# Optimization experiments

Measured on AMD Instinct MI355X. Metric: run time of the kernel, lower is better.

## Reference

```python
import jax, jax.numpy as jnp
import numpy as np

NUM_CLASSES = 80
GRID = 13
A = 9                      # 3 scales x 3 anchors, flattened
P = GRID * GRID * A        # 1521 priors
OBJ_SCALE, NOOBJ_SCALE, CLS_SCALE, BOX_SCALE = 1.0, 100.0, 1.0, 5.0
ANCHORS_NP = np.array([[10,13],[16,30],[33,23],[30,61],[62,45],[59,119],[116,90],[156,198],[373,326]], dtype=np.float32)


def setup_inputs() -> dict:
    key = jax.random.key(0)
    k1, k2, k3, k4, k5 = jax.random.split(key, 5)
    B, T = 512, 50
    predictions = jax.random.normal(k1, (B, P, 5 + NUM_CLASSES), dtype=jnp.float32)
    xy = jax.random.uniform(k2, (B, T, 2), minval=0.02, maxval=0.98)
    wh = jax.random.uniform(k3, (B, T, 2), minval=0.01, maxval=0.30)
    conf = (jax.random.uniform(k4, (B, T, 1)) < 0.6).astype(jnp.float32)
    cls = jax.random.randint(k5, (B, T, 1), 0, NUM_CLASSES).astype(jnp.float32)
    targets = jnp.concatenate([xy, wh, conf, cls], axis=-1)  # [B,T,6]
    anchors = jnp.asarray(ANCHORS_NP)                        # [9,2]
    return {"predictions": predictions, "targets": targets, "anchors": anchors}


def _safe_log(x):
    # torch BCELoss clamps log terms at -100
    return jnp.maximum(jnp.log(x), -100.0)


def _per_image(pred, tgt, anchors):
    # pred: [P, 5+C], tgt: [T, 6], anchors: [A, 2]
    valid = tgt[:, 4] > 0
    has = jnp.any(valid)
    # wh-only IoU: target wh scaled by 1000 (pixel scale) vs anchor wh
    tw_px = tgt[:, 2] * 1000.0
    th_px = tgt[:, 3] * 1000.0
    aw = anchors[:, 0][:, None]  # [A,1]
    ah = anchors[:, 1][:, None]
    inter = jnp.minimum(aw, tw_px[None, :]) * jnp.minimum(ah, th_px[None, :])  # [A,T]
    union = aw * ah + tw_px * th_px - inter
    iou = inter / (union + 1e-16)
    best_a = jnp.argmax(iou, axis=0)  # [T]
    gx = jnp.floor(tgt[:, 0] * GRID).astype(jnp.int32)
    gy = jnp.floor(tgt[:, 1] * GRID).astype(jnp.int32)
    prior = gy * (GRID * A) + gx * A + best_a
    prior = jnp.where(valid, prior, P)  # invalid targets scatter out-of-range -> dropped

    obj = jnp.zeros((P,), jnp.float32).at[prior].set(1.0, mode='drop')
    txv = tgt[:, 0] * GRID - gx.astype(jnp.float32)
    tyv = tgt[:, 1] * GRID - gy.astype(jnp.float32)
    aw_b = anchors[best_a, 0]
    ah_b = anchors[best_a, 1]
    twv = jnp.log(tgt[:, 2] * GRID / aw_b + 1e-16)
    thv = jnp.log(tgt[:, 3] * GRID / ah_b + 1e-16)
    tx = jnp.zeros((P,), jnp.float32).at[prior].set(txv, mode='drop')
    ty = jnp.zeros((P,), jnp.float32).at[prior].set(tyv, mode='drop')
    tw = jnp.zeros((P,), jnp.float32).at[prior].set(twv, mode='drop')
    th = jnp.zeros((P,), jnp.float32).at[prior].set(thv, mode='drop')
    cls_idx = tgt[:, 5].astype(jnp.int32)
    tcls = jnp.zeros((P, NUM_CLASSES), jnp.float32).at[prior, cls_idx].set(1.0, mode='drop')

    conf_p = jax.nn.sigmoid(pred[:, 4])
    logp = _safe_log(conf_p)
    log1mp = _safe_log(1.0 - conf_p)

    box = BOX_SCALE * jnp.sum(obj * ((pred[:, 0] - tx) ** 2 + (pred[:, 1] - ty) ** 2
                                     + (pred[:, 2] - tw) ** 2 + (pred[:, 3] - th) ** 2))
    objl = -OBJ_SCALE * jnp.sum(obj * logp)
    # empty-image branch: BCE(conf, ones).sum() = -sum(log p); otherwise BCE over noobj priors vs 0
    noobjl = jnp.where(has,
                       -NOOBJ_SCALE * jnp.sum((1.0 - obj) * log1mp),
                       -NOOBJ_SCALE * jnp.sum(logp))
    pcls = jax.nn.sigmoid(pred[:, 5:])
    bce_cls = -(tcls * _safe_log(pcls) + (1.0 - tcls) * _safe_log(1.0 - pcls))
    clsl = CLS_SCALE * jnp.sum(obj[:, None] * bce_cls)
    return box, objl, noobjl, clsl


def reference(predictions, targets, anchors):
    box, objl, noobjl, clsl = jax.vmap(lambda p, t: _per_image(p, t, anchors))(predictions, targets)
    B = predictions.shape[0]
    box_loss = jnp.sum(box) / B
    obj_loss = jnp.sum(objl) / B
    noobj_loss = jnp.sum(noobjl) / B
    cls_loss = jnp.sum(clsl) / B
    total = box_loss + obj_loss + noobj_loss + cls_loss
    return (total, box_loss, obj_loss, noobj_loss, cls_loss)
```

## Files before the change

kernel.cpp:

```cpp
#include <hip/hip_runtime.h>
#include <cmath>

#define B_N 512
#define T_N 50
#define GRIDN 13
#define A_N 9
#define P_N 1521
#define ROW 85
#define NCLS 80

struct Entry {
    int prior;
    float tx, ty, tw, th;
    unsigned int cls[3];
};

__global__ void __launch_bounds__(256)
main_kernel(const float* __restrict__ pred,
            const float* __restrict__ tgt,
            const float* __restrict__ anchors,
            float* __restrict__ part)
{
    __shared__ Entry ents[T_N];
    __shared__ int   s_cnt;
    __shared__ float red[4][5];

    const int tid  = threadIdx.x;
    const int lane = tid & 63;
    const int b    = blockIdx.x;

    if (tid < 64) {
        int   prior = -1;
        float txv = 0.f, tyv = 0.f, twv = 0.f, thv = 0.f;
        int   cls = 0;

        if (lane < T_N) {
            const float* t = tgt + ((size_t)b * T_N + lane) * 6;
            float x = t[0], y = t[1], w = t[2], h = t[3], conf = t[4];
            if (conf > 0.0f) {
                float tw_px = w * 1000.0f, th_px = h * 1000.0f;
                int best = 0; float bestv = -1.0f;
                #pragma unroll
                for (int a = 0; a < A_N; ++a) {
                    float aw = anchors[2*a], ah = anchors[2*a+1];
                    float inter = fminf(aw, tw_px) * fminf(ah, th_px);
                    float uni   = aw*ah + tw_px*th_px - inter;
                    float iou   = inter / (uni + 1e-16f);
                    if (iou > bestv) { bestv = iou; best = a; }
                }
                int gx = (int)floorf(x * (float)GRIDN);
                int gy = (int)floorf(y * (float)GRIDN);
                prior = gy * (GRIDN * A_N) + gx * A_N + best;
                txv = x * (float)GRIDN - (float)gx;
                tyv = y * (float)GRIDN - (float)gy;
                float aw = anchors[2*best], ah = anchors[2*best+1];
                twv = logf(w * (float)GRIDN / aw + 1e-16f);
                thv = logf(h * (float)GRIDN / ah + 1e-16f);
                cls = (int)t[5];
            }
        }

        bool valid = (prior >= 0);
        unsigned int m0 = 0, m1 = 0, m2 = 0;
        bool laterdup = false;
        #pragma unroll
        for (int j = 0; j < T_N; ++j) {
            int pj = __shfl(prior, j, 64);
            int cj = __shfl(cls,   j, 64);
            if (valid && pj == prior) {
                if (j > lane) laterdup = true;
                if (cj < 32)      m0 |= 1u << cj;
                else if (cj < 64) m1 |= 1u << (cj - 32);
                else              m2 |= 1u << (cj - 64);
            }
        }
        bool winner = valid && !laterdup;
        unsigned long long mask = __ballot(winner);
        if (winner) {
            int idx = __popcll(mask & ((1ull << lane) - 1ull));
            Entry* e = &ents[idx];
            e->prior = prior;
            e->tx = txv; e->ty = tyv; e->tw = twv; e->th = thv;
            e->cls[0] = m0; e->cls[1] = m1; e->cls[2] = m2;
        }
        if (lane == 0) s_cnt = __popcll(mask);
    }
    __syncthreads();

    const int  cnt  = s_cnt;
    const bool hasv = (cnt > 0);

    const float* pb = pred + (size_t)b * P_N * ROW;
    float s_main = 0.0f;
    #pragma unroll
    for (int p = tid; p < P_N; p += 256) {
        float x = pb[(size_t)p * ROW + 4];
        float s = 1.0f / (1.0f + __expf(-x));
        float v = hasv ? fmaxf(__logf(1.0f - s), -100.0f)
                       : fmaxf(__logf(s),        -100.0f);
        s_main += v;
    }

    float cls_s = 0.0f, box_s = 0.0f, objlp = 0.0f, objl1 = 0.0f;
    {
        const int half = tid >> 7;
        const int lt   = tid & 127;
        for (int e = half; e < cnt; e += 2) {
            Entry en = ents[e];
            const float* row = pb + (size_t)en.prior * ROW;
            if (lt < NCLS) {
                float x  = row[5 + lt];
                float s  = 1.0f / (1.0f + __expf(-x));
                float lp = fmaxf(__logf(s),        -100.0f);
                float l1 = fmaxf(__logf(1.0f - s), -100.0f);
                float tc = ((en.cls[lt >> 5] >> (lt & 31)) & 1u) ? 1.0f : 0.0f;
                cls_s += -(tc * lp + (1.0f - tc) * l1);
            } else if (lt == NCLS) {
                float x = row[4];
                float s = 1.0f / (1.0f + __expf(-x));
                objlp += fmaxf(__logf(s),        -100.0f);
                objl1 += fmaxf(__logf(1.0f - s), -100.0f);
            } else if (lt == NCLS + 1) {
                float d0 = row[0] - en.tx;
                float d1 = row[1] - en.ty;
                float d2 = row[2] - en.tw;
                float d3 = row[3] - en.th;
                box_s += d0*d0 + d1*d1 + d2*d2 + d3*d3;
            }
        }
    }

    float v0 = s_main, v1 = objl1, v2 = objlp, v3 = box_s, v4 = cls_s;
    #pragma unroll
    for (int o = 32; o > 0; o >>= 1) {
        v0 += __shfl_down(v0, o, 64);
        v1 += __shfl_down(v1, o, 64);
        v2 += __shfl_down(v2, o, 64);
        v3 += __shfl_down(v3, o, 64);
        v4 += __shfl_down(v4, o, 64);
    }
    const int w = tid >> 6;
    if (lane == 0) {
        red[w][0] = v0; red[w][1] = v1; red[w][2] = v2;
        red[w][3] = v3; red[w][4] = v4;
    }
    __syncthreads();
    if (tid == 0) {
        float S  = red[0][0] + red[1][0] + red[2][0] + red[3][0];
        float L1 = red[0][1] + red[1][1] + red[2][1] + red[3][1];
        float LP = red[0][2] + red[1][2] + red[2][2] + red[3][2];
        float BX = red[0][3] + red[1][3] + red[2][3] + red[3][3];
        float CL = red[0][4] + red[1][4] + red[2][4] + red[3][4];
        float* o = part + (size_t)b * 4;
        o[0] = 5.0f * BX;
        o[1] = -LP;
        o[2] = -100.0f * (S - L1);
        o[3] = CL;
    }
}

__global__ void __launch_bounds__(256)
finalize_kernel(const float* __restrict__ part, float* __restrict__ out)
{
    __shared__ float red[4][4];
    const int tid  = threadIdx.x;
    const int lane = tid & 63;

    float a0 = 0, a1 = 0, a2 = 0, a3 = 0;
    for (int b = tid; b < B_N; b += 256) {
        const float* p = part + (size_t)b * 4;
        a0 += p[0]; a1 += p[1]; a2 += p[2]; a3 += p[3];
    }
    #pragma unroll
    for (int o = 32; o > 0; o >>= 1) {
        a0 += __shfl_down(a0, o, 64);
        a1 += __shfl_down(a1, o, 64);
        a2 += __shfl_down(a2, o, 64);
        a3 += __shfl_down(a3, o, 64);
    }
    const int w = tid >> 6;
    if (lane == 0) { red[w][0] = a0; red[w][1] = a1; red[w][2] = a2; red[w][3] = a3; }
    __syncthreads();
    if (tid == 0) {
        const float invB = 1.0f / (float)B_N;
        float box   = (red[0][0] + red[1][0] + red[2][0] + red[3][0]) * invB;
        float obj   = (red[0][1] + red[1][1] + red[2][1] + red[3][1]) * invB;
        float noobj = (red[0][2] + red[1][2] + red[2][2] + red[3][2]) * invB;
        float cls   = (red[0][3] + red[1][3] + red[2][3] + red[3][3]) * invB;
        out[0] = box + obj + noobj + cls;
        out[1] = box;
        out[2] = obj;
        out[3] = noobj;
        out[4] = cls;
    }
}

extern "C" void kernel_launch(void* const* d_in, const int* in_sizes, int n_in,
                              void* d_out, int out_size, void* d_ws, size_t ws_size,
                              hipStream_t stream)
{
    const float* pred    = (const float*)d_in[0];
    const float* tgt     = (const float*)d_in[1];
    const float* anchors = (const float*)d_in[2];
    float* out  = (float*)d_out;
    float* part = (float*)d_ws;

    main_kernel<<<dim3(B_N), dim3(256), 0, stream>>>(pred, tgt, anchors, part);
    finalize_kernel<<<dim3(1), dim3(256), 0, stream>>>(part, out);
}
```

Before: 52.65 us.

## Split per-image prior sweep across four blocks per image

Launches a 2D grid with four blocks per image. Each block sums the noobj log terms over its own slice of the 1521 priors. Only chunk 0 builds the target entries and computes the class, box and obj corrections; the other chunks only check whether the image has any valid target. Partial sums go to separate workspace arrays, which the finalize kernel combines, so the strided conf-column gather gets more parallelism and occupancy at the cost of redundant target reads and more blocks.

New measurement: 66.82 us. +26.9%, slower.

```diff
diff --git a/kernel.cpp b/kernel.cpp
--- a/kernel.cpp
+++ b/kernel.cpp
@@ -8,6 +8,8 @@
 #define P_N 1521
 #define ROW 85
 #define NCLS 80
+#define CHUNKS 4
+#define CH_P 381
 
 struct Entry {
     int prior;
@@ -19,71 +21,78 @@
 main_kernel(const float* __restrict__ pred,
             const float* __restrict__ tgt,
             const float* __restrict__ anchors,
-            float* __restrict__ part)
+            float* __restrict__ S_part,
+            float* __restrict__ corr)
 {
     __shared__ Entry ents[T_N];
+    __shared__ float red[4][5];
     __shared__ int   s_cnt;
-    __shared__ float red[4][5];
-
-    const int tid  = threadIdx.x;
-    const int lane = tid & 63;
-    const int b    = blockIdx.x;
+
+    const int  tid  = threadIdx.x;
+    const int  lane = tid & 63;
+    const int  b    = blockIdx.y;
+    const int  c    = blockIdx.x;
+    const bool isc0 = (c == 0);
 
     if (tid < 64) {
-        int   prior = -1;
-        float txv = 0.f, tyv = 0.f, twv = 0.f, thv = 0.f;
-        int   cls = 0;
-
-        if (lane < T_N) {
-            const float* t = tgt + ((size_t)b * T_N + lane) * 6;
-            float x = t[0], y = t[1], w = t[2], h = t[3], conf = t[4];
-            if (conf > 0.0f) {
-                float tw_px = w * 1000.0f, th_px = h * 1000.0f;
-                int best = 0; float bestv = -1.0f;
-                #pragma unroll
-                for (int a = 0; a < A_N; ++a) {
-                    float aw = anchors[2*a], ah = anchors[2*a+1];
-                    float inter = fminf(aw, tw_px) * fminf(ah, th_px);
-                    float uni   = aw*ah + tw_px*th_px - inter;
-                    float iou   = inter / (uni + 1e-16f);
-                    if (iou > bestv) { bestv = iou; best = a; }
+        if (isc0) {
+            int   prior = -1;
+            float txv = 0.f, tyv = 0.f, twv = 0.f, thv = 0.f;
+            int   cls = 0;
+            if (lane < T_N) {
+                const float* t = tgt + ((size_t)b * T_N + lane) * 6;
+                float x = t[0], y = t[1], w = t[2], h = t[3], conf = t[4];
+                if (conf > 0.0f) {
+                    float tw_px = w * 1000.0f, th_px = h * 1000.0f;
+                    int best = 0; float bestv = -1.0f;
+                    #pragma unroll
+                    for (int a = 0; a < A_N; ++a) {
+                        float aw = anchors[2*a], ah = anchors[2*a+1];
+                        float inter = fminf(aw, tw_px) * fminf(ah, th_px);
+                        float uni   = aw*ah + tw_px*th_px - inter;
+                        float iou   = inter / (uni + 1e-16f);
+                        if (iou > bestv) { bestv = iou; best = a; }
+                    }
+                    int gx = (int)floorf(x * (float)GRIDN);
+                    int gy = (int)floorf(y * (float)GRIDN);
+                    prior = gy * (GRIDN * A_N) + gx * A_N + best;
+                    txv = x * (float)GRIDN - (float)gx;
+                    tyv = y * (float)GRIDN - (float)gy;
+                    float aw = anchors[2*best], ah = anchors[2*best+1];
+                    twv = logf(w * (float)GRIDN / aw + 1e-16f);
+                    thv = logf(h * (float)GRIDN / ah + 1e-16f);
+                    cls = (int)t[5];
                 }
-                int gx = (int)floorf(x * (float)GRIDN);
-                int gy = (int)floorf(y * (float)GRIDN);
-                prior = gy * (GRIDN * A_N) + gx * A_N + best;
-                txv = x * (float)GRIDN - (float)gx;
-                tyv = y * (float)GRIDN - (float)gy;
-                float aw = anchors[2*best], ah = anchors[2*best+1];
-                twv = logf(w * (float)GRIDN / aw + 1e-16f);
-                thv = logf(h * (float)GRIDN / ah + 1e-16f);
-                cls = (int)t[5];
-            }
+            }
+            bool valid = (prior >= 0);
+            unsigned int m0 = 0, m1 = 0, m2 = 0;
+            bool laterdup = false;
+            #pragma unroll
+            for (int j = 0; j < T_N; ++j) {
+                int pj = __shfl(prior, j, 64);
+                int cj = __shfl(cls,   j, 64);
+                if (valid && pj == prior) {
+                    if (j > lane) laterdup = true;
+                    if (cj < 32)      m0 |= 1u << cj;
+                    else if (cj < 64) m1 |= 1u << (cj - 32);
+                    else              m2 |= 1u << (cj - 64);
+                }
+            }
+            bool winner = valid && !laterdup;
+            unsigned long long mask = __ballot(winner);
+            if (winner) {
+                int idx = __popcll(mask & ((1ull << lane) - 1ull));
+                Entry* e = &ents[idx];
+                e->prior = prior;
+                e->tx = txv; e->ty = tyv; e->tw = twv; e->th = thv;
+                e->cls[0] = m0; e->cls[1] = m1; e->cls[2] = m2;
+            }
+            if (lane == 0) s_cnt = __popcll(mask);
+        } else {
+            float conf = (lane < T_N) ? tgt[((size_t)b * T_N + lane) * 6 + 4] : 0.0f;
+            unsigned long long m = __ballot(conf > 0.0f);
+            if (lane == 0) s_cnt = (m != 0ull) ? 1 : 0;
         }
-
-        bool valid = (prior >= 0);
-        unsigned int m0 = 0, m1 = 0, m2 = 0;
-        bool laterdup = false;
-        #pragma unroll
-        for (int j = 0; j < T_N; ++j) {
-            int pj = __shfl(prior, j, 64);
-            int cj = __shfl(cls,   j, 64);
-            if (valid && pj == prior) {
-                if (j > lane) laterdup = true;
-                if (cj < 32)      m0 |= 1u << cj;
-                else if (cj < 64) m1 |= 1u << (cj - 32);
-                else              m2 |= 1u << (cj - 64);
-            }
-        }
-        bool winner = valid && !laterdup;
-        unsigned long long mask = __ballot(winner);
-        if (winner) {
-            int idx = __popcll(mask & ((1ull << lane) - 1ull));
-            Entry* e = &ents[idx];
-            e->prior = prior;
-            e->tx = txv; e->ty = tyv; e->tw = twv; e->th = thv;
-            e->cls[0] = m0; e->cls[1] = m1; e->cls[2] = m2;
-        }
-        if (lane == 0) s_cnt = __popcll(mask);
     }
     __syncthreads();
 
@@ -91,18 +100,18 @@
     const bool hasv = (cnt > 0);
 
     const float* pb = pred + (size_t)b * P_N * ROW;
+    const int p0 = c * CH_P;
+    const int p1 = (p0 + CH_P < P_N) ? p0 + CH_P : P_N;
     float s_main = 0.0f;
-    #pragma unroll
-    for (int p = tid; p < P_N; p += 256) {
+    for (int p = p0 + tid; p < p1; p += 256) {
         float x = pb[(size_t)p * ROW + 4];
         float s = 1.0f / (1.0f + __expf(-x));
-        float v = hasv ? fmaxf(__logf(1.0f - s), -100.0f)
+        s_main += hasv ? fmaxf(__logf(1.0f - s), -100.0f)
                        : fmaxf(__logf(s),        -100.0f);
-        s_main += v;
     }
 
     float cls_s = 0.0f, box_s = 0.0f, objlp = 0.0f, objl1 = 0.0f;
-    {
+    if (isc0) {
         const int half = tid >> 7;
         const int lt   = tid & 127;
         for (int e = half; e < cnt; e += 2) {
@@ -146,40 +155,47 @@
     }
     __syncthreads();
     if (tid == 0) {
-        float S  = red[0][0] + red[1][0] + red[2][0] + red[3][0];
-        float L1 = red[0][1] + red[1][1] + red[2][1] + red[3][1];
-        float LP = red[0][2] + red[1][2] + red[2][2] + red[3][2];
-        float BX = red[0][3] + red[1][3] + red[2][3] + red[3][3];
-        float CL = red[0][4] + red[1][4] + red[2][4] + red[3][4];
-        float* o = part + (size_t)b * 4;
-        o[0] = 5.0f * BX;
-        o[1] = -LP;
-        o[2] = -100.0f * (S - L1);
-        o[3] = CL;
+        float S = red[0][0] + red[1][0] + red[2][0] + red[3][0];
+        S_part[(b << 2) + c] = S;
+        if (isc0) {
+            float L1 = red[0][1] + red[1][1] + red[2][1] + red[3][1];
+            float LP = red[0][2] + red[1][2] + red[2][2] + red[3][2];
+            float BX = red[0][3] + red[1][3] + red[2][3] + red[3][3];
+            float CL = red[0][4] + red[1][4] + red[2][4] + red[3][4];
+            float* o = corr + (size_t)b * 4;
+            o[0] = BX; o[1] = LP; o[2] = L1; o[3] = CL;
+        }
     }
 }
 
 __global__ void __launch_bounds__(256)
-finalize_kernel(const float* __restrict__ part, float* __restrict__ out)
+finalize_kernel(const float* __restrict__ S_part,
+                const float* __restrict__ corr,
+                float* __restrict__ out)
 {
     __shared__ float red[4][4];
     const int tid  = threadIdx.x;
     const int lane = tid & 63;
 
-    float a0 = 0, a1 = 0, a2 = 0, a3 = 0;
+    float a_box = 0, a_obj = 0, a_noobj = 0, a_cls = 0;
     for (int b = tid; b < B_N; b += 256) {
-        const float* p = part + (size_t)b * 4;
-        a0 += p[0]; a1 += p[1]; a2 += p[2]; a3 += p[3];
+        float4 s4 = ((const float4*)S_part)[b];
+        float  S  = (s4.x + s4.y) + (s4.z + s4.w);
+        float4 cr = ((const float4*)corr)[b];
+        a_box   += 5.0f * cr.x;
+        a_obj   += -cr.y;
+        a_noobj += -100.0f * (S - cr.z);
+        a_cls   += cr.w;
     }
     #pragma unroll
     for (int o = 32; o > 0; o >>= 1) {
-        a0 += __shfl_down(a0, o, 64);
-        a1 += __shfl_down(a1, o, 64);
-        a2 += __shfl_down(a2, o, 64);
-        a3 += __shfl_down(a3, o, 64);
+        a_box   += __shfl_down(a_box,   o, 64);
+        a_obj   += __shfl_down(a_obj,   o, 64);
+        a_noobj += __shfl_down(a_noobj, o, 64);
+        a_cls   += __shfl_down(a_cls,   o, 64);
     }
     const int w = tid >> 6;
-    if (lane == 0) { red[w][0] = a0; red[w][1] = a1; red[w][2] = a2; red[w][3] = a3; }
+    if (lane == 0) { red[w][0] = a_box; red[w][1] = a_obj; red[w][2] = a_noobj; red[w][3] = a_cls; }
     __syncthreads();
     if (tid == 0) {
         const float invB = 1.0f / (float)B_N;
@@ -202,9 +218,12 @@
     const float* pred    = (const float*)d_in[0];
     const float* tgt     = (const float*)d_in[1];
     const float* anchors = (const float*)d_in[2];
-    float* out  = (float*)d_out;
-    float* part = (float*)d_ws;
-
-    main_kernel<<<dim3(B_N), dim3(256), 0, stream>>>(pred, tgt, anchors, part);
-    finalize_kernel<<<dim3(1), dim3(256), 0, stream>>>(part, out);
+    float* out = (float*)d_out;
+
+    char*  ws     = (char*)d_ws;
+    float* S_part = (float*)ws;
+    float* corr   = (float*)(ws + 8192);
+
+    main_kernel<<<dim3(CHUNKS, B_N), dim3(256), 0, stream>>>(pred, tgt, anchors, S_part, corr);
+    finalize_kernel<<<dim3(1), dim3(256), 0, stream>>>(S_part, corr, out);
 }
```

## Stream whole prediction slab with float4 loads and widen blocks to 1024 threads

Applied to the files above, without the earlier changes.

The per-image conf sum now reads the entire prediction slab with aligned float4 loads and picks the conf column by modulo, instead of doing strided scalar loads of one float per row. The has-target flag is computed up front with a ballot so this streaming can start before the target preprocessing and first barrier. Blocks grow to 1024 threads (16 waves) with 8 entry groups, and the final loss combination moves into the finalize kernel. This reads about 85x more bytes per image in exchange for coalesced vector loads. A partial float4 at the slab end is skipped, which appears harmless only because the tail row's conf element falls inside a full float4.

After: 54.72 us. 3.9% more time.

```diff
diff --git a/kernel.cpp b/kernel.cpp
--- a/kernel.cpp
+++ b/kernel.cpp
@@ -8,6 +8,8 @@
 #define P_N 1521
 #define ROW 85
 #define NCLS 80
+#define FPI (P_N * ROW)
+#define NTHR 1024
 
 struct Entry {
     int prior;
@@ -15,7 +17,7 @@
     unsigned int cls[3];
 };
 
-__global__ void __launch_bounds__(256)
+__global__ void __launch_bounds__(NTHR)
 main_kernel(const float* __restrict__ pred,
             const float* __restrict__ tgt,
             const float* __restrict__ anchors,
@@ -23,19 +25,40 @@
 {
     __shared__ Entry ents[T_N];
     __shared__ int   s_cnt;
-    __shared__ float red[4][5];
+    __shared__ float red[16][5];
 
     const int tid  = threadIdx.x;
     const int lane = tid & 63;
     const int b    = blockIdx.x;
+
+    const float* tb = tgt + (size_t)b * T_N * 6;
+    float confv = (lane < T_N) ? tb[lane * 6 + 4] : 0.0f;
+    const bool hasv = (__ballot(confv > 0.0f) != 0ull);
+
+    const float* slab = pred + (size_t)b * FPI;
+    const int a0 = (4 - (b & 3)) & 3;
+    const int NQ = (FPI - a0) >> 2;
+    const float4* qp = (const float4*)(slab + a0);
+    float s_main = 0.0f;
+    for (int q = tid; q < NQ; q += NTHR) {
+        float4 v = qp[q];
+        int f0 = a0 + (q << 2);
+        int c0 = f0 % 85;
+        if ((unsigned)(c0 - 1) <= 3u) {
+            int k = 4 - c0;
+            float x = (k == 0) ? v.x : (k == 1) ? v.y : (k == 2) ? v.z : v.w;
+            float s = 1.0f / (1.0f + __expf(-x));
+            s_main += hasv ? fmaxf(__logf(1.0f - s), -100.0f)
+                           : fmaxf(__logf(s),        -100.0f);
+        }
+    }
 
     if (tid < 64) {
         int   prior = -1;
         float txv = 0.f, tyv = 0.f, twv = 0.f, thv = 0.f;
         int   cls = 0;
-
         if (lane < T_N) {
-            const float* t = tgt + ((size_t)b * T_N + lane) * 6;
+            const float* t = tb + lane * 6;
             float x = t[0], y = t[1], w = t[2], h = t[3], conf = t[4];
             if (conf > 0.0f) {
                 float tw_px = w * 1000.0f, th_px = h * 1000.0f;
@@ -59,7 +82,6 @@
                 cls = (int)t[5];
             }
         }
-
         bool valid = (prior >= 0);
         unsigned int m0 = 0, m1 = 0, m2 = 0;
         bool laterdup = false;
@@ -87,27 +109,15 @@
     }
     __syncthreads();
 
-    const int  cnt  = s_cnt;
-    const bool hasv = (cnt > 0);
-
-    const float* pb = pred + (size_t)b * P_N * ROW;
-    float s_main = 0.0f;
-    #pragma unroll
-    for (int p = tid; p < P_N; p += 256) {
-        float x = pb[(size_t)p * ROW + 4];
-        float s = 1.0f / (1.0f + __expf(-x));
-        float v = hasv ? fmaxf(__logf(1.0f - s), -100.0f)
-                       : fmaxf(__logf(s),        -100.0f);
-        s_main += v;
-    }
+    const int cnt = s_cnt;
 
     float cls_s = 0.0f, box_s = 0.0f, objlp = 0.0f, objl1 = 0.0f;
     {
-        const int half = tid >> 7;
-        const int lt   = tid & 127;
-        for (int e = half; e < cnt; e += 2) {
+        const int gid = tid >> 7;
+        const int lt  = tid & 127;
+        for (int e = gid; e < cnt; e += 8) {
             Entry en = ents[e];
-            const float* row = pb + (size_t)en.prior * ROW;
+            const float* row = slab + (size_t)en.prior * ROW;
             if (lt < NCLS) {
                 float x  = row[5 + lt];
                 float s  = 1.0f / (1.0f + __expf(-x));
@@ -145,17 +155,11 @@
         red[w][3] = v3; red[w][4] = v4;
     }
     __syncthreads();
-    if (tid == 0) {
-        float S  = red[0][0] + red[1][0] + red[2][0] + red[3][0];
-        float L1 = red[0][1] + red[1][1] + red[2][1] + red[3][1];
-        float LP = red[0][2] + red[1][2] + red[2][2] + red[3][2];
-        float BX = red[0][3] + red[1][3] + red[2][3] + red[3][3];
-        float CL = red[0][4] + red[1][4] + red[2][4] + red[3][4];
-        float* o = part + (size_t)b * 4;
-        o[0] = 5.0f * BX;
-        o[1] = -LP;
-        o[2] = -100.0f * (S - L1);
-        o[3] = CL;
+    if (tid < 5) {
+        float s = 0.0f;
+        #pragma unroll
+        for (int ww = 0; ww < 16; ++ww) s += red[ww][tid];
+        part[(size_t)b * 5 + tid] = s;
     }
 }
 
@@ -166,20 +170,28 @@
     const int tid  = threadIdx.x;
     const int lane = tid & 63;
 
-    float a0 = 0, a1 = 0, a2 = 0, a3 = 0;
+    float a_box = 0, a_obj = 0, a_noobj = 0, a_cls = 0;
     for (int b = tid; b < B_N; b += 256) {
-        const float* p = part + (size_t)b * 4;
-        a0 += p[0]; a1 += p[1]; a2 += p[2]; a3 += p[3];
+        const float* p = part + (size_t)b * 5;
+        float S  = p[0];
+        float L1 = p[1];
+        float LP = p[2];
+        float BX = p[3];
+        float CL = p[4];
+        a_box   += 5.0f * BX;
+        a_obj   += -LP;
+        a_noobj += -100.0f * (S - L1);
+        a_cls   += CL;
     }
     #pragma unroll
     for (int o = 32; o > 0; o >>= 1) {
-        a0 += __shfl_down(a0, o, 64);
-        a1 += __shfl_down(a1, o, 64);
-        a2 += __shfl_down(a2, o, 64);
-        a3 += __shfl_down(a3, o, 64);
+        a_box   += __shfl_down(a_box,   o, 64);
+        a_obj   += __shfl_down(a_obj,   o, 64);
+        a_noobj += __shfl_down(a_noobj, o, 64);
+        a_cls   += __shfl_down(a_cls,   o, 64);
     }
     const int w = tid >> 6;
-    if (lane == 0) { red[w][0] = a0; red[w][1] = a1; red[w][2] = a2; red[w][3] = a3; }
+    if (lane == 0) { red[w][0] = a_box; red[w][1] = a_obj; red[w][2] = a_noobj; red[w][3] = a_cls; }
     __syncthreads();
     if (tid == 0) {
         const float invB = 1.0f / (float)B_N;
@@ -205,6 +217,6 @@
     float* out  = (float*)d_out;
     float* part = (float*)d_ws;
 
-    main_kernel<<<dim3(B_N), dim3(256), 0, stream>>>(pred, tgt, anchors, part);
+    main_kernel<<<dim3(B_N), dim3(NTHR), 0, stream>>>(pred, tgt, anchors, part);
     finalize_kernel<<<dim3(1), dim3(256), 0, stream>>>(part, out);
 }
```
